# Optimization experiments

Measured on AMD Instinct MI355X. Metric: run time of the kernel, lower is better.

The kernel has to match this reference:

```python
import jax, jax.numpy as jnp
import numpy as np

B, C, H, W = 8, 512, 32, 32
NH, DH = 8, 64            # n_head, d_head = C // n_head
L = 2                     # n_layer
NC, DC = 77, 768          # n_cond, d_cond
GROUPS = 32


def _layernorm(x, s, b, eps=1e-5):
    mu = jnp.mean(x, axis=-1, keepdims=True)
    var = jnp.var(x, axis=-1, keepdims=True)
    return (x - mu) * jax.lax.rsqrt(var + eps) * s + b


def _groupnorm(x, s, b, eps=1e-6):
    # x: (B,C,H,W) -> 32 groups over channels
    b_, c_, h_, w_ = x.shape
    xg = x.reshape(b_, GROUPS, c_ // GROUPS, h_, w_)
    mu = jnp.mean(xg, axis=(2, 3, 4), keepdims=True)
    var = jnp.var(xg, axis=(2, 3, 4), keepdims=True)
    xg = (xg - mu) * jax.lax.rsqrt(var + eps)
    return xg.reshape(b_, c_, h_, w_) * s[None, :, None, None] + b[None, :, None, None]


def _attention(x, kv, wq, wk, wv, wo, bo):
    # NOTE: source's normal_attention applies NO 1/sqrt(d) scale (faithful).
    bsz, sq, _ = x.shape
    sk = kv.shape[1]
    q = (x @ wq).reshape(bsz, sq, NH, DH)
    k = (kv @ wk).reshape(bsz, sk, NH, DH)
    v = (kv @ wv).reshape(bsz, sk, NH, DH)
    attn = jnp.einsum('bind,bjnd->bnij', q, k)
    attn = jax.nn.softmax(attn, axis=-1)
    out = jnp.einsum('bnij,bjnd->bind', attn, v).reshape(bsz, sq, NH * DH)
    return out @ wo + bo


def setup_inputs() -> dict:
    key = jax.random.key(0)
    ks = iter(jax.random.split(key, 40))
    rn = lambda *shape: jax.random.normal(next(ks), shape, dtype=jnp.float32) * 0.02
    d = {
        'x': jax.random.normal(next(ks), (B, C, H, W), dtype=jnp.float32),
        'cond': jax.random.normal(next(ks), (B, NC, DC), dtype=jnp.float32),
        'gn_s': jnp.ones((C,), jnp.float32), 'gn_b': jnp.zeros((C,), jnp.float32),
        'pin_w': rn(C, C), 'pin_b': jnp.zeros((C,), jnp.float32),
        'pout_w': rn(C, C), 'pout_b': jnp.zeros((C,), jnp.float32),
        # per-layer (stacked along leading L dim)
        'ln1_s': jnp.ones((L, C), jnp.float32), 'ln1_b': jnp.zeros((L, C), jnp.float32),
        'sa_wq': rn(L, C, C), 'sa_wk': rn(L, C, C), 'sa_wv': rn(L, C, C),
        'sa_wo': rn(L, C, C), 'sa_bo': jnp.zeros((L, C), jnp.float32),
        'ln2_s': jnp.ones((L, C), jnp.float32), 'ln2_b': jnp.zeros((L, C), jnp.float32),
        'ca_wq': rn(L, C, C), 'ca_wk': rn(L, DC, C), 'ca_wv': rn(L, DC, C),
        'ca_wo': rn(L, C, C), 'ca_bo': jnp.zeros((L, C), jnp.float32),
        'ln3_s': jnp.ones((L, C), jnp.float32), 'ln3_b': jnp.zeros((L, C), jnp.float32),
        'ff_w1': rn(L, C, 8 * C), 'ff_b1': jnp.zeros((L, 8 * C), jnp.float32),
        'ff_w2': rn(L, 4 * C, C), 'ff_b2': jnp.zeros((L, C), jnp.float32),
    }
    return d


def reference(x, cond, gn_s, gn_b, pin_w, pin_b, pout_w, pout_b,
              ln1_s, ln1_b, sa_wq, sa_wk, sa_wv, sa_wo, sa_bo,
              ln2_s, ln2_b, ca_wq, ca_wk, ca_wv, ca_wo, ca_bo,
              ln3_s, ln3_b, ff_w1, ff_b1, ff_w2, ff_b2):
    b, c, h, w = x.shape
    x_in = x
    xn = _groupnorm(x, gn_s, gn_b)
    # 1x1 conv == per-pixel linear
    xn = jnp.einsum('bchw,cd->bdhw', xn, pin_w) + pin_b[None, :, None, None]
    t = xn.transpose(0, 2, 3, 1).reshape(b, h * w, c)  # b (h w) c
    for i in range(L):
        t = _attention(_layernorm(t, ln1_s[i], ln1_b[i]), _layernorm(t, ln1_s[i], ln1_b[i]),
                       sa_wq[i], sa_wk[i], sa_wv[i], sa_wo[i], sa_bo[i]) + t
        t = _attention(_layernorm(t, ln2_s[i], ln2_b[i]), cond,
                       ca_wq[i], ca_wk[i], ca_wv[i], ca_wo[i], ca_bo[i]) + t
        hgate = _layernorm(t, ln3_s[i], ln3_b[i]) @ ff_w1[i] + ff_b1[i]
        u, gate = jnp.split(hgate, 2, axis=-1)
        t = (u * jax.nn.gelu(gate, approximate=False)) @ ff_w2[i] + ff_b2[i] + t
    y = t.reshape(b, h, w, c).transpose(0, 3, 1, 2)
    y = jnp.einsum('bchw,cd->bdhw', y, pout_w) + pout_b[None, :, None, None]
    return y + x_in
```

## Files before the change

kernel.cpp:

```cpp
#include <hip/hip_runtime.h>
#include <math.h>

static constexpr int Bn  = 8;
static constexpr int Cn  = 512;
static constexpr int HWn = 1024;
static constexpr int Sn  = 1024;
static constexpr int NCn = 77;
static constexpr int NCp = 640;
static constexpr int DCn = 768;

typedef unsigned short u16;
typedef __attribute__((ext_vector_type(8))) short short8v;
typedef __attribute__((ext_vector_type(4))) float f32x4;
typedef __attribute__((ext_vector_type(8))) unsigned short u16x8;

__device__ __forceinline__ u16 f2b(float f) {
  unsigned u = __float_as_uint(f);
  return (u16)((u + 0x7fffu + ((u >> 16) & 1u)) >> 16);
}
__device__ __forceinline__ float b2f(u16 h) {
  return __uint_as_float(((unsigned)h) << 16);
}

#define GLDS16(gp, lp) __builtin_amdgcn_global_load_lds( \
    (const __attribute__((address_space(1))) void*)(gp),  \
    (__attribute__((address_space(3))) void*)(lp), 16, 0, 0)

__global__ __launch_bounds__(256) void w_cast_t(const float* __restrict__ in,
    u16* __restrict__ out, int K, int N)
{
  __shared__ float tile[32][33];
  int k0 = blockIdx.x * 32, n0 = blockIdx.y * 32;
  int px = threadIdx.x & 31, py = threadIdx.x >> 5;
  for (int yy = py; yy < 32; yy += 8)
    tile[yy][px] = in[(size_t)(k0 + yy) * N + n0 + px];
  __syncthreads();
  for (int yy = py; yy < 32; yy += 8)
    out[(size_t)(n0 + yy) * K + k0 + px] = f2b(tile[px][yy]);
}

__global__ __launch_bounds__(256) void cond_cast(const float* __restrict__ in,
    u16* __restrict__ out)
{
  int idx = blockIdx.x * 256 + threadIdx.x;
  int m = idx / DCn;
  out[idx] = (m < Bn * NCn) ? f2b(in[idx]) : (u16)0;
}

__global__ __launch_bounds__(256) void cast_f2b8(const float* __restrict__ in,
    u16* __restrict__ out)
{
  int i = blockIdx.x * 256 + threadIdx.x;
  const float4* p = (const float4*)(in + (size_t)i * 8);
  float4 a = p[0], b = p[1];
  u16x8 o;
  o[0] = f2b(a.x); o[1] = f2b(a.y); o[2] = f2b(a.z); o[3] = f2b(a.w);
  o[4] = f2b(b.x); o[5] = f2b(b.y); o[6] = f2b(b.z); o[7] = f2b(b.w);
  *(u16x8*)(out + (size_t)i * 8) = o;
}

__global__ __launch_bounds__(256) void gn_kernel(const float* __restrict__ x,
    const float* __restrict__ gs, const float* __restrict__ gb, float* __restrict__ out)
{
  int b = blockIdx.x >> 5, g = blockIdx.x & 31;
  const float* xp = x + ((size_t)b * Cn + g * 16) * HWn;
  float s = 0.f, ss = 0.f;
  for (int e = threadIdx.x; e < 16 * HWn; e += 256) {
    float v = xp[e];
    s += v; ss += v * v;
  }
  __shared__ float red[10];
  #pragma unroll
  for (int o = 32; o; o >>= 1) { s += __shfl_xor(s, o, 64); ss += __shfl_xor(ss, o, 64); }
  if ((threadIdx.x & 63) == 0) { red[threadIdx.x >> 6] = s; red[(threadIdx.x >> 6) + 4] = ss; }
  __syncthreads();
  if (threadIdx.x == 0) {
    float st  = red[0] + red[1] + red[2] + red[3];
    float sst = red[4] + red[5] + red[6] + red[7];
    float mu  = st * (1.f / 16384.f);
    red[8] = mu;
    red[9] = rsqrtf(sst * (1.f / 16384.f) - mu * mu + 1e-6f);
  }
  __syncthreads();
  float mu = red[8], inv = red[9];
  float* op = out + ((size_t)b * Cn + g * 16) * HWn;
  for (int e = threadIdx.x; e < 16 * HWn; e += 256) {
    int cl = e >> 10;
    op[e] = (xp[e] - mu) * inv * gs[g * 16 + cl] + gb[g * 16 + cl];
  }
}

__global__ __launch_bounds__(256) void gn_t_cast(const float* __restrict__ in,
    u16* __restrict__ out)
{
  __shared__ float tile[32][33];
  int p0 = blockIdx.x * 32, c0 = blockIdx.y * 32, b = blockIdx.z;
  int px = threadIdx.x & 31, py = threadIdx.x >> 5;
  for (int yy = py; yy < 32; yy += 8)
    tile[yy][px] = in[((size_t)b * Cn + c0 + yy) * HWn + p0 + px];
  __syncthreads();
  for (int yy = py; yy < 32; yy += 8)
    out[((size_t)b * HWn + p0 + yy) * Cn + c0 + px] = f2b(tile[px][yy]);
}

__global__ __launch_bounds__(256) void ln_kernel(const float* __restrict__ in,
    const float* __restrict__ s, const float* __restrict__ b, u16* __restrict__ out)
{
  int row  = blockIdx.x * 4 + (threadIdx.x >> 6);
  int lane = threadIdx.x & 63;
  const float* ip = in + (size_t)row * Cn + lane * 8;
  float4 v0 = *(const float4*)ip;
  float4 v1 = *(const float4*)(ip + 4);
  float sum = v0.x + v0.y + v0.z + v0.w + v1.x + v1.y + v1.z + v1.w;
  float ss  = v0.x*v0.x + v0.y*v0.y + v0.z*v0.z + v0.w*v0.w
            + v1.x*v1.x + v1.y*v1.y + v1.z*v1.z + v1.w*v1.w;
  #pragma unroll
  for (int o = 32; o; o >>= 1) { sum += __shfl_xor(sum, o, 64); ss += __shfl_xor(ss, o, 64); }
  float mu  = sum * (1.f / Cn);
  float inv = rsqrtf(ss * (1.f / Cn) - mu * mu + 1e-5f);
  const float4 s0 = *(const float4*)(s + lane * 8);
  const float4 s1 = *(const float4*)(s + lane * 8 + 4);
  const float4 b0 = *(const float4*)(b + lane * 8);
  const float4 b1 = *(const float4*)(b + lane * 8 + 4);
  u16x8 o;
  o[0] = f2b((v0.x - mu) * inv * s0.x + b0.x);
  o[1] = f2b((v0.y - mu) * inv * s0.y + b0.y);
  o[2] = f2b((v0.z - mu) * inv * s0.z + b0.z);
  o[3] = f2b((v0.w - mu) * inv * s0.w + b0.w);
  o[4] = f2b((v1.x - mu) * inv * s1.x + b1.x);
  o[5] = f2b((v1.y - mu) * inv * s1.y + b1.y);
  o[6] = f2b((v1.z - mu) * inv * s1.z + b1.z);
  o[7] = f2b((v1.w - mu) * inv * s1.w + b1.w);
  *(u16x8*)(out + (size_t)row * Cn + lane * 8) = o;
}

template<int EPI, int OUT>
__global__ __launch_bounds__(256) void gemm_mfma(const u16* __restrict__ A,
    const u16* __restrict__ Bt, const float* __restrict__ bias,
    const float* __restrict__ res, void* __restrict__ outp, int M, int K, int N)
{
  __shared__ __align__(16) u16 As[128 * 32];
  __shared__ __align__(16) u16 Bs[128 * 32];
  int tid = threadIdx.x, lane = tid & 63, wid = tid >> 6;
  int n0 = blockIdx.x * 128, m0 = blockIdx.y * 128;
  int wr = wid >> 1, wc = wid & 1;
  int r16 = lane & 15, q4 = lane >> 4;
  f32x4 acc[4][4] = {};
  for (int k0 = 0; k0 < K; k0 += 32) {
    #pragma unroll
    for (int i = 0; i < 2; i++) {
      int c = wid * 128 + i * 64 + lane;
      size_t ldso = (size_t)(wid * 2 + i) * 1024;
      GLDS16(A  + (size_t)(m0 + (c >> 2)) * K + k0 + (c & 3) * 8, (char*)As + ldso);
      GLDS16(Bt + (size_t)(n0 + (c >> 2)) * K + k0 + (c & 3) * 8, (char*)Bs + ldso);
    }
    __syncthreads();
    short8v a[4], b[4];
    #pragma unroll
    for (int m = 0; m < 4; m++)
      a[m] = *(const short8v*)((const char*)As + (wr * 64 + m * 16 + r16) * 64 + q4 * 16);
    #pragma unroll
    for (int n = 0; n < 4; n++)
      b[n] = *(const short8v*)((const char*)Bs + (wc * 64 + n * 16 + r16) * 64 + q4 * 16);
    #pragma unroll
    for (int m = 0; m < 4; m++)
      #pragma unroll
      for (int n = 0; n < 4; n++)
        acc[m][n] = __builtin_amdgcn_mfma_f32_16x16x32_bf16(a[m], b[n], acc[m][n], 0, 0, 0);
    __syncthreads();
  }
  #pragma unroll
  for (int m = 0; m < 4; m++) {
    int gm0 = m0 + wr * 64 + m * 16 + q4 * 4;
    #pragma unroll
    for (int n = 0; n < 4; n++) {
      int gc = n0 + wc * 64 + n * 16 + r16;
      float bv = (EPI >= 1) ? bias[gc] : 0.f;
      if (OUT == 2) {
        int bb = gm0 >> 10, s0 = gm0 & 1023;
        ushort4 pk;
        pk.x = f2b(acc[m][n][0] + bv);
        pk.y = f2b(acc[m][n][1] + bv);
        pk.z = f2b(acc[m][n][2] + bv);
        pk.w = f2b(acc[m][n][3] + bv);
        *(ushort4*)((u16*)outp + ((size_t)bb * Cn + gc) * (size_t)Sn + s0) = pk;
      } else {
        #pragma unroll
        for (int r = 0; r < 4; r++) {
          float v = acc[m][n][r] + bv;
          size_t oi = (size_t)(gm0 + r) * N + gc;
          if (EPI == 2) v += res[oi];
          if (OUT == 0) ((float*)outp)[oi] = v;
          else          ((u16*)outp)[oi]   = f2b(v);
        }
      }
    }
  }
}

__global__ __launch_bounds__(256) void ff_gate_mfma(const u16* __restrict__ A,
    const u16* __restrict__ W1t, const float* __restrict__ bias,
    u16* __restrict__ out, int M, int K)
{
  __shared__ __align__(16) u16 As[128 * 32];
  __shared__ __align__(16) u16 Bu[128 * 32];
  __shared__ __align__(16) u16 Bg[128 * 32];
  int tid = threadIdx.x, lane = tid & 63, wid = tid >> 6;
  int n0 = blockIdx.x * 128, m0 = blockIdx.y * 128;
  int wr = wid >> 1, wc = wid & 1;
  int r16 = lane & 15, q4 = lane >> 4;
  f32x4 au[4][4] = {}, ag[4][4] = {};
  for (int k0 = 0; k0 < K; k0 += 32) {
    #pragma unroll
    for (int i = 0; i < 2; i++) {
      int c = wid * 128 + i * 64 + lane;
      size_t ldso = (size_t)(wid * 2 + i) * 1024;
      int row = c >> 2, sub = (c & 3) * 8;
      GLDS16(A   + (size_t)(m0 + row) * K + k0 + sub,          (char*)As + ldso);
      GLDS16(W1t + (size_t)(n0 + row) * K + k0 + sub,          (char*)Bu + ldso);
      GLDS16(W1t + (size_t)(2048 + n0 + row) * K + k0 + sub,   (char*)Bg + ldso);
    }
    __syncthreads();
    short8v a[4], bu[4], bg[4];
    #pragma unroll
    for (int m = 0; m < 4; m++)
      a[m] = *(const short8v*)((const char*)As + (wr * 64 + m * 16 + r16) * 64 + q4 * 16);
    #pragma unroll
    for (int n = 0; n < 4; n++) {
      bu[n] = *(const short8v*)((const char*)Bu + (wc * 64 + n * 16 + r16) * 64 + q4 * 16);
      bg[n] = *(const short8v*)((const char*)Bg + (wc * 64 + n * 16 + r16) * 64 + q4 * 16);
    }
    #pragma unroll
    for (int m = 0; m < 4; m++)
      #pragma unroll
      for (int n = 0; n < 4; n++) {
        au[m][n] = __builtin_amdgcn_mfma_f32_16x16x32_bf16(a[m], bu[n], au[m][n], 0, 0, 0);
        ag[m][n] = __builtin_amdgcn_mfma_f32_16x16x32_bf16(a[m], bg[n], ag[m][n], 0, 0, 0);
      }
    __syncthreads();
  }
  #pragma unroll
  for (int m = 0; m < 4; m++) {
    int gm0 = m0 + wr * 64 + m * 16 + q4 * 4;
    #pragma unroll
    for (int n = 0; n < 4; n++) {
      int gc = n0 + wc * 64 + n * 16 + r16;
      float bu_ = bias[gc], bg_ = bias[2048 + gc];
      #pragma unroll
      for (int r = 0; r < 4; r++) {
        float u = au[m][n][r] + bu_;
        float g = ag[m][n][r] + bg_;
        float ge = 0.5f * g * (1.f + erff(g * 0.70710678118f));
        out[(size_t)(gm0 + r) * 2048 + gc] = f2b(u * ge);
      }
    }
  }
}

__global__ __launch_bounds__(256) void attn_self_mfma(const u16* __restrict__ q,
    const u16* __restrict__ k, const u16* __restrict__ vt, u16* __restrict__ o)
{
  __shared__ __align__(16) u16 Qs[64 * 64];
  __shared__ __align__(16) u16 Ks[2][64 * 64];
  __shared__ __align__(16) u16 Vs[2][64 * 64];
  __shared__ __align__(16) u16 Ps[4 * 16 * 64];
  int tid = threadIdx.x, lane = tid & 63, wid = tid >> 6;
  int r16 = lane & 15, q4 = lane >> 4;
  int qt = blockIdx.x & 15, h = (blockIdx.x >> 4) & 7, b = blockIdx.x >> 7;

  const u16* qg = q  + ((size_t)(b * Sn + qt * 64)) * Cn + h * 64;
  const u16* kg = k  + ((size_t)b * Sn) * Cn + h * 64;
  const u16* vg = vt + ((size_t)(b * Cn + h * 64)) * Sn;

  #define STAGE_T(dst, gbase, rs) do { \
    _Pragma("unroll") \
    for (int ii = 0; ii < 2; ii++) { \
      int rr = ii * 32 + wid * 8 + (lane >> 3); \
      GLDS16((gbase) + (size_t)rr * (rs) + (((lane & 7) ^ (rr & 7)) << 3), \
             (char*)(dst) + ii * 4096 + wid * 1024); \
    } \
  } while (0)

  STAGE_T(Qs, qg, Cn);
  STAGE_T(Ks[0], kg, Cn);
  STAGE_T(Vs[0], vg, Sn);
  __syncthreads();

  short8v aq[2];
  {
    int qrow = wid * 16 + r16, sx = r16 & 7;
    const char* base = (const char*)Qs + qrow * 128;
    aq[0] = *(const short8v*)(base + ((q4 ^ sx) << 4));
    aq[1] = *(const short8v*)(base + (((4 | q4) ^ sx) << 4));
  }

  float m_r[4] = {-1e30f, -1e30f, -1e30f, -1e30f};
  float l_r[4] = {0.f, 0.f, 0.f, 0.f};
  f32x4 acc_o[4] = {};
  int cur = 0;
  char* pwave = (char*)Ps + wid * 2048;

  for (int t = 0; t < 16; t++) {
    if (t < 15) {
      STAGE_T(Ks[cur ^ 1], kg + (size_t)(t + 1) * 64 * Cn, Cn);
      STAGE_T(Vs[cur ^ 1], vg + (t + 1) * 64, Sn);
    }
    f32x4 s4[4];
    #pragma unroll
    for (int n = 0; n < 4; n++) {
      int krow = n * 16 + r16, sx = r16 & 7;
      const char* base = (const char*)Ks[cur] + krow * 128;
      short8v b0 = *(const short8v*)(base + ((q4 ^ sx) << 4));
      short8v b1 = *(const short8v*)(base + (((4 | q4) ^ sx) << 4));
      f32x4 z = {0.f, 0.f, 0.f, 0.f};
      z = __builtin_amdgcn_mfma_f32_16x16x32_bf16(aq[0], b0, z, 0, 0, 0);
      s4[n] = __builtin_amdgcn_mfma_f32_16x16x32_bf16(aq[1], b1, z, 0, 0, 0);
    }
    #pragma unroll
    for (int r = 0; r < 4; r++) {
      float tm = fmaxf(fmaxf(s4[0][r], s4[1][r]), fmaxf(s4[2][r], s4[3][r]));
      #pragma unroll
      for (int off = 8; off; off >>= 1) tm = fmaxf(tm, __shfl_xor(tm, off, 64));
      float mn = fmaxf(m_r[r], tm);
      float al = __expf(m_r[r] - mn);
      m_r[r] = mn;
      int prow = q4 * 4 + r;
      char* pbase = pwave + prow * 128;
      int sx = (prow & 7) << 4;
      float rs = 0.f;
      #pragma unroll
      for (int n = 0; n < 4; n++) {
        float p = __expf(s4[n][r] - mn);
        rs += p;
        int cb = ((((n << 4) | r16) << 1) ^ sx);
        *(u16*)(pbase + cb) = f2b(p);
      }
      #pragma unroll
      for (int off = 8; off; off >>= 1) rs += __shfl_xor(rs, off, 64);
      l_r[r] = l_r[r] * al + rs;
      #pragma unroll
      for (int n = 0; n < 4; n++) acc_o[n][r] *= al;
    }
    __syncthreads();
    short8v pa0, pa1;
    {
      int sx = r16 & 7;
      const char* base = pwave + r16 * 128;
      pa0 = *(const short8v*)(base + ((q4 ^ sx) << 4));
      pa1 = *(const short8v*)(base + (((4 | q4) ^ sx) << 4));
    }
    #pragma unroll
    for (int n = 0; n < 4; n++) {
      int vrow = n * 16 + r16, sx = r16 & 7;
      const char* base = (const char*)Vs[cur] + vrow * 128;
      short8v v0 = *(const short8v*)(base + ((q4 ^ sx) << 4));
      short8v v1 = *(const short8v*)(base + (((4 | q4) ^ sx) << 4));
      acc_o[n] = __builtin_amdgcn_mfma_f32_16x16x32_bf16(pa0, v0, acc_o[n], 0, 0, 0);
      acc_o[n] = __builtin_amdgcn_mfma_f32_16x16x32_bf16(pa1, v1, acc_o[n], 0, 0, 0);
    }
    __syncthreads();
    cur ^= 1;
  }

  u16* ob = o + ((size_t)(b * Sn + qt * 64 + wid * 16 + q4 * 4)) * Cn + h * 64;
  #pragma unroll
  for (int r = 0; r < 4; r++) {
    float inv = 1.f / l_r[r];
    #pragma unroll
    for (int n = 0; n < 4; n++)
      ob[(size_t)r * Cn + n * 16 + r16] = f2b(acc_o[n][r] * inv);
  }
  #undef STAGE_T
}

__global__ __launch_bounds__(256) void vt_cross_k(const u16* __restrict__ v,
    u16* __restrict__ vt)
{
  int c = blockIdx.x * 256 + threadIdx.x;
  int b = blockIdx.y;
  u16* op = vt + ((size_t)b * Cn + c) * 96;
  for (int j = 0; j < 96; j++)
    op[j] = (j < NCn) ? v[((size_t)b * NCn + j) * Cn + c] : (u16)0;
}

__global__ __launch_bounds__(256) void attn_cross_mfma(const u16* __restrict__ q,
    const u16* __restrict__ k, const u16* __restrict__ vt, u16* __restrict__ o)
{
  __shared__ __align__(16) u16 Ps[4][16 * 104];
  int tid = threadIdx.x, lane = tid & 63, wid = tid >> 6;
  int r16 = lane & 15, q4 = lane >> 4;
  int qt = blockIdx.x & 15, h = (blockIdx.x >> 4) & 7, b = blockIdx.x >> 7;

  const u16* qg = q + ((size_t)(b * Sn + qt * 64 + wid * 16 + r16)) * Cn + h * 64 + q4 * 8;
  short8v aq0 = *(const short8v*)qg;
  short8v aq1 = *(const short8v*)(qg + 32);

  f32x4 s[6];
  #pragma unroll
  for (int n = 0; n < 6; n++) {
    const u16* kr = k + ((size_t)(b * NCn + n * 16 + r16)) * Cn + h * 64 + q4 * 8;
    short8v b0 = *(const short8v*)kr;
    short8v b1 = *(const short8v*)(kr + 32);
    f32x4 z = {0.f, 0.f, 0.f, 0.f};
    z = __builtin_amdgcn_mfma_f32_16x16x32_bf16(aq0, b0, z, 0, 0, 0);
    s[n] = __builtin_amdgcn_mfma_f32_16x16x32_bf16(aq1, b1, z, 0, 0, 0);
  }
  #pragma unroll
  for (int n = 0; n < 6; n++)
    if (n * 16 + r16 >= NCn) {
      s[n][0] = -1e30f; s[n][1] = -1e30f; s[n][2] = -1e30f; s[n][3] = -1e30f;
    }

  float l_r[4];
  u16* pw = &Ps[wid][0];
  #pragma unroll
  for (int r = 0; r < 4; r++) {
    float tm = -1e30f;
    #pragma unroll
    for (int n = 0; n < 6; n++) tm = fmaxf(tm, s[n][r]);
    #pragma unroll
    for (int off = 8; off; off >>= 1) tm = fmaxf(tm, __shfl_xor(tm, off, 64));
    int prow = q4 * 4 + r;
    float rs = 0.f;
    #pragma unroll
    for (int n = 0; n < 6; n++) {
      float p = __expf(s[n][r] - tm);
      rs += p;
      pw[prow * 104 + n * 16 + r16] = f2b(p);
    }
    #pragma unroll
    for (int off = 8; off; off >>= 1) rs += __shfl_xor(rs, off, 64);
    l_r[r] = rs;
  }
  __syncthreads();

  short8v pa[3];
  #pragma unroll
  for (int c = 0; c < 3; c++)
    pa[c] = *(const short8v*)(pw + r16 * 104 + c * 32 + q4 * 8);
  f32x4 acc[4] = {};
  #pragma unroll
  for (int n = 0; n < 4; n++) {
    const u16* vr = vt + ((size_t)(b * Cn + h * 64 + n * 16 + r16)) * 96;
    #pragma unroll
    for (int c = 0; c < 3; c++) {
      short8v bv = *(const short8v*)(vr + c * 32 + q4 * 8);
      acc[n] = __builtin_amdgcn_mfma_f32_16x16x32_bf16(pa[c], bv, acc[n], 0, 0, 0);
    }
  }

  u16* ob = o + ((size_t)(b * Sn + qt * 64 + wid * 16 + q4 * 4)) * Cn + h * 64;
  #pragma unroll
  for (int r = 0; r < 4; r++) {
    float inv = 1.f / l_r[r];
    #pragma unroll
    for (int n = 0; n < 4; n++)
      ob[(size_t)r * Cn + n * 16 + r16] = f2b(acc[n][r] * inv);
  }
}

__global__ __launch_bounds__(256) void trans_add(const float* __restrict__ tin,
    const float* __restrict__ pb, const float* __restrict__ xin, float* __restrict__ out)
{
  __shared__ float tile[32][33];
  int p0 = blockIdx.x * 32, d0 = blockIdx.y * 32, b = blockIdx.z;
  int px = threadIdx.x & 31, py = threadIdx.x >> 5;
  for (int yy = py; yy < 32; yy += 8)
    tile[yy][px] = tin[((size_t)b * HWn + p0 + yy) * Cn + d0 + px];
  __syncthreads();
  for (int yy = py; yy < 32; yy += 8) {
    int dd = d0 + yy;
    size_t oidx = ((size_t)b * Cn + dd) * HWn + p0 + px;
    out[oidx] = tile[px][yy] + pb[dd] + xin[oidx];
  }
}

extern "C" void kernel_launch(void* const* d_in, const int* in_sizes, int n_in,
                              void* d_out, int out_size, void* d_ws, size_t ws_size,
                              hipStream_t stream) {
  const float* x      = (const float*)d_in[0];
  const float* cond   = (const float*)d_in[1];
  const float* gn_s   = (const float*)d_in[2];
  const float* gn_b   = (const float*)d_in[3];
  const float* pin_w  = (const float*)d_in[4];
  const float* pin_b  = (const float*)d_in[5];
  const float* pout_w = (const float*)d_in[6];
  const float* pout_b = (const float*)d_in[7];
  const float* ln1_s  = (const float*)d_in[8];
  const float* ln1_b  = (const float*)d_in[9];
  const float* sa_wq  = (const float*)d_in[10];
  const float* sa_wk  = (const float*)d_in[11];
  const float* sa_wv  = (const float*)d_in[12];
  const float* sa_wo  = (const float*)d_in[13];
  const float* sa_bo  = (const float*)d_in[14];
  const float* ln2_s  = (const float*)d_in[15];
  const float* ln2_b  = (const float*)d_in[16];
  const float* ca_wq  = (const float*)d_in[17];
  const float* ca_wk  = (const float*)d_in[18];
  const float* ca_wv  = (const float*)d_in[19];
  const float* ca_wo  = (const float*)d_in[20];
  const float* ca_bo  = (const float*)d_in[21];
  const float* ln3_s  = (const float*)d_in[22];
  const float* ln3_b  = (const float*)d_in[23];
  const float* ff_w1  = (const float*)d_in[24];
  const float* ff_b1  = (const float*)d_in[25];
  const float* ff_w2  = (const float*)d_in[26];
  const float* ff_b2  = (const float*)d_in[27];

  const int M = Bn * Sn;
  const size_t MB = 1ull << 20;
  char* ws = (char*)d_ws;
  float* t     = (float*)(ws);
  u16*   abf   = (u16*)  (ws + 16 * MB);
  float* qb    = (float*)(ws + 24 * MB);
  float* kb    = (float*)(ws + 40 * MB);
  float* vb    = (float*)(ws + 56 * MB);
  u16*   hb    = (u16*)  (ws + 72 * MB);
  float* gnout = (float*)(ws + 72 * MB);
  u16*   xb    = (u16*)  (ws + 88 * MB);
  u16*   vtc   = (u16*)  (ws + 96 * MB);
  u16*   condb = (u16*)  (ws + 104 * MB);
  u16*   wts   = (u16*)  (ws + 105 * MB);

  u16* q16  = (u16*)qb;
  u16* k16  = (u16*)kb;
  u16* v16  = (u16*)vb;
  u16* vt16 = (u16*)vb;

  u16* wp = wts;
  u16* pinT  = wp; wp += 512 * 512;
  u16* poutT = wp; wp += 512 * 512;
  u16 *sa_wqT[2], *sa_wkT[2], *sa_wvT[2], *sa_woT[2];
  u16 *ca_wqT[2], *ca_wkT[2], *ca_wvT[2], *ca_woT[2], *ff_w1T[2], *ff_w2T[2];
  for (int i = 0; i < 2; i++) {
    sa_wqT[i] = wp; wp += 512 * 512;
    sa_wkT[i] = wp; wp += 512 * 512;
    sa_wvT[i] = wp; wp += 512 * 512;
    sa_woT[i] = wp; wp += 512 * 512;
    ca_wqT[i] = wp; wp += 512 * 512;
    ca_wkT[i] = wp; wp += 768 * 512;
    ca_wvT[i] = wp; wp += 768 * 512;
    ca_woT[i] = wp; wp += 512 * 512;
    ff_w1T[i] = wp; wp += 512 * 4096;
    ff_w2T[i] = wp; wp += 2048 * 512;
  }

  dim3 tcc(16, 16);
  w_cast_t<<<tcc, 256, 0, stream>>>(pin_w, pinT, 512, 512);
  w_cast_t<<<tcc, 256, 0, stream>>>(pout_w, poutT, 512, 512);
  for (int i = 0; i < 2; i++) {
    const size_t wCC = (size_t)i * 512 * 512, wDC = (size_t)i * 768 * 512;
    w_cast_t<<<tcc, 256, 0, stream>>>(sa_wq + wCC, sa_wqT[i], 512, 512);
    w_cast_t<<<tcc, 256, 0, stream>>>(sa_wk + wCC, sa_wkT[i], 512, 512);
    w_cast_t<<<tcc, 256, 0, stream>>>(sa_wv + wCC, sa_wvT[i], 512, 512);
    w_cast_t<<<tcc, 256, 0, stream>>>(sa_wo + wCC, sa_woT[i], 512, 512);
    w_cast_t<<<tcc, 256, 0, stream>>>(ca_wq + wCC, ca_wqT[i], 512, 512);
    w_cast_t<<<dim3(24, 16), 256, 0, stream>>>(ca_wk + wDC, ca_wkT[i], 768, 512);
    w_cast_t<<<dim3(24, 16), 256, 0, stream>>>(ca_wv + wDC, ca_wvT[i], 768, 512);
    w_cast_t<<<tcc, 256, 0, stream>>>(ca_wo + wCC, ca_woT[i], 512, 512);
    w_cast_t<<<dim3(16, 128), 256, 0, stream>>>(ff_w1 + (size_t)i * 512 * 4096, ff_w1T[i], 512, 4096);
    w_cast_t<<<dim3(64, 16), 256, 0, stream>>>(ff_w2 + (size_t)i * 2048 * 512, ff_w2T[i], 2048, 512);
  }
  cond_cast<<<(NCp * DCn) / 256, 256, 0, stream>>>(cond, condb);

  gn_kernel<<<256, 256, 0, stream>>>(x, gn_s, gn_b, gnout);
  gn_t_cast<<<dim3(32, 16, 8), 256, 0, stream>>>(gnout, xb);
  gemm_mfma<1, 0><<<dim3(4, 64), 256, 0, stream>>>(xb, pinT, pin_b, nullptr, t, M, 512, 512);

  for (int i = 0; i < 2; i++) {
    ln_kernel<<<2048, 256, 0, stream>>>(t, ln1_s + i * Cn, ln1_b + i * Cn, abf);
    gemm_mfma<0, 1><<<dim3(4, 64), 256, 0, stream>>>(abf, sa_wqT[i], nullptr, nullptr, q16, M, 512, 512);
    gemm_mfma<0, 1><<<dim3(4, 64), 256, 0, stream>>>(abf, sa_wkT[i], nullptr, nullptr, k16, M, 512, 512);
    gemm_mfma<0, 2><<<dim3(4, 64), 256, 0, stream>>>(abf, sa_wvT[i], nullptr, nullptr, vt16, M, 512, 512);
    attn_self_mfma<<<1024, 256, 0, stream>>>(q16, k16, vt16, abf);
    gemm_mfma<2, 0><<<dim3(4, 64), 256, 0, stream>>>(abf, sa_woT[i], sa_bo + i * Cn, t, t, M, 512, 512);
    ln_kernel<<<2048, 256, 0, stream>>>(t, ln2_s + i * Cn, ln2_b + i * Cn, abf);
    gemm_mfma<0, 1><<<dim3(4, 64), 256, 0, stream>>>(abf, ca_wqT[i], nullptr, nullptr, q16, M, 512, 512);
    gemm_mfma<0, 1><<<dim3(4, 5), 256, 0, stream>>>(condb, ca_wkT[i], nullptr, nullptr, k16, NCp, 768, 512);
    gemm_mfma<0, 1><<<dim3(4, 5), 256, 0, stream>>>(condb, ca_wvT[i], nullptr, nullptr, v16, NCp, 768, 512);
    vt_cross_k<<<dim3(2, 8), 256, 0, stream>>>(v16, vtc);
    attn_cross_mfma<<<1024, 256, 0, stream>>>(q16, k16, vtc, abf);
    gemm_mfma<2, 0><<<dim3(4, 64), 256, 0, stream>>>(abf, ca_woT[i], ca_bo + i * Cn, t, t, M, 512, 512);
    ln_kernel<<<2048, 256, 0, stream>>>(t, ln3_s + i * Cn, ln3_b + i * Cn, abf);
    ff_gate_mfma<<<dim3(16, 64), 256, 0, stream>>>(abf, ff_w1T[i], ff_b1 + i * 4096, hb, M, 512);
    gemm_mfma<2, 0><<<dim3(4, 64), 256, 0, stream>>>(hb, ff_w2T[i], ff_b2 + i * Cn, t, t, M, 2048, 512);
  }

  cast_f2b8<<<2048, 256, 0, stream>>>(t, xb);
  gemm_mfma<0, 0><<<dim3(4, 64), 256, 0, stream>>>(xb, poutT, nullptr, nullptr, qb, M, 512, 512);
  trans_add<<<dim3(32, 16, 8), 256, 0, stream>>>(qb, pout_b, x, (float*)d_out);
}
```

Baseline: 1.123 ms.

## Fuse QKV and cross-KV GEMMs, add 64-row tile variant, use fast erf

Merges the three self-attention projection GEMMs into one N=1536 launch whose epilogue routes columns to q, k and transposed v. It likewise merges the cross-attention K and V projections into one N=1024 launch. Both rely on the transposed weight buffers sitting contiguously in memory. The 512-wide GEMMs switch to a 64-row M tile, doubling the grid to better fill the CUs. The library erff in the GEGLU epilogue is replaced with an Abramowitz-Stegun polynomial plus exp, which adds a small approximation error.

```diff
diff --git a/kernel.cpp b/kernel.cpp
--- a/kernel.cpp
+++ b/kernel.cpp
@@ -20,6 +20,14 @@
 }
 __device__ __forceinline__ float b2f(u16 h) {
   return __uint_as_float(((unsigned)h) << 16);
+}
+__device__ __forceinline__ float erf_as(float x) {
+  float ax = fabsf(x);
+  float t  = 1.f / (1.f + 0.3275911f * ax);
+  float y  = t * (0.254829592f + t * (-0.284496736f + t * (1.421413741f +
+             t * (-1.453152027f + t * 1.061405429f))));
+  float r  = 1.f - y * __expf(-ax * ax);
+  return copysignf(r, x);
 }
 
 #define GLDS16(gp, lp) __builtin_amdgcn_global_load_lds( \
@@ -134,44 +142,57 @@
   *(u16x8*)(out + (size_t)row * Cn + lane * 8) = o;
 }
 
-template<int EPI, int OUT>
+template<int EPI, int OUT, int MT>
 __global__ __launch_bounds__(256) void gemm_mfma(const u16* __restrict__ A,
     const u16* __restrict__ Bt, const float* __restrict__ bias,
-    const float* __restrict__ res, void* __restrict__ outp, int M, int K, int N)
-{
-  __shared__ __align__(16) u16 As[128 * 32];
+    const float* __restrict__ res, void* __restrict__ outp,
+    void* __restrict__ out2, void* __restrict__ out3, int M, int K, int N)
+{
+  constexpr int MFR = MT / 32;
+  __shared__ __align__(16) u16 As[MT * 32];
   __shared__ __align__(16) u16 Bs[128 * 32];
   int tid = threadIdx.x, lane = tid & 63, wid = tid >> 6;
-  int n0 = blockIdx.x * 128, m0 = blockIdx.y * 128;
+  int n0 = blockIdx.x * 128, m0 = blockIdx.y * MT;
   int wr = wid >> 1, wc = wid & 1;
   int r16 = lane & 15, q4 = lane >> 4;
-  f32x4 acc[4][4] = {};
+  f32x4 acc[MFR][4] = {};
   for (int k0 = 0; k0 < K; k0 += 32) {
+    if (MT == 128) {
+      #pragma unroll
+      for (int i = 0; i < 2; i++) {
+        int c = wid * 128 + i * 64 + lane;
+        GLDS16(A + (size_t)(m0 + (c >> 2)) * K + k0 + (c & 3) * 8,
+               (char*)As + (size_t)(wid * 2 + i) * 1024);
+      }
+    } else {
+      int c = tid;
+      GLDS16(A + (size_t)(m0 + (c >> 2)) * K + k0 + (c & 3) * 8,
+             (char*)As + (size_t)wid * 1024);
+    }
     #pragma unroll
     for (int i = 0; i < 2; i++) {
       int c = wid * 128 + i * 64 + lane;
-      size_t ldso = (size_t)(wid * 2 + i) * 1024;
-      GLDS16(A  + (size_t)(m0 + (c >> 2)) * K + k0 + (c & 3) * 8, (char*)As + ldso);
-      GLDS16(Bt + (size_t)(n0 + (c >> 2)) * K + k0 + (c & 3) * 8, (char*)Bs + ldso);
+      GLDS16(Bt + (size_t)(n0 + (c >> 2)) * K + k0 + (c & 3) * 8,
+             (char*)Bs + (size_t)(wid * 2 + i) * 1024);
     }
     __syncthreads();
-    short8v a[4], b[4];
-    #pragma unroll
-    for (int m = 0; m < 4; m++)
-      a[m] = *(const short8v*)((const char*)As + (wr * 64 + m * 16 + r16) * 64 + q4 * 16);
+    short8v a[MFR], b[4];
+    #pragma unroll
+    for (int m = 0; m < MFR; m++)
+      a[m] = *(const short8v*)((const char*)As + (wr * (MT / 2) + m * 16 + r16) * 64 + q4 * 16);
     #pragma unroll
     for (int n = 0; n < 4; n++)
       b[n] = *(const short8v*)((const char*)Bs + (wc * 64 + n * 16 + r16) * 64 + q4 * 16);
     #pragma unroll
-    for (int m = 0; m < 4; m++)
+    for (int m = 0; m < MFR; m++)
       #pragma unroll
       for (int n = 0; n < 4; n++)
         acc[m][n] = __builtin_amdgcn_mfma_f32_16x16x32_bf16(a[m], b[n], acc[m][n], 0, 0, 0);
     __syncthreads();
   }
   #pragma unroll
-  for (int m = 0; m < 4; m++) {
-    int gm0 = m0 + wr * 64 + m * 16 + q4 * 4;
+  for (int m = 0; m < MFR; m++) {
+    int gm0 = m0 + wr * (MT / 2) + m * 16 + q4 * 4;
     #pragma unroll
     for (int n = 0; n < 4; n++) {
       int gc = n0 + wc * 64 + n * 16 + r16;
@@ -184,6 +205,26 @@
         pk.z = f2b(acc[m][n][2] + bv);
         pk.w = f2b(acc[m][n][3] + bv);
         *(ushort4*)((u16*)outp + ((size_t)bb * Cn + gc) * (size_t)Sn + s0) = pk;
+      } else if (OUT == 3) {
+        if (gc < 1024) {
+          u16* dst = (gc < 512) ? (u16*)outp : (u16*)out2;
+          int cc = gc & 511;
+          #pragma unroll
+          for (int r = 0; r < 4; r++)
+            dst[(size_t)(gm0 + r) * Cn + cc] = f2b(acc[m][n][r]);
+        } else {
+          int bb = gm0 >> 10, s0 = gm0 & 1023, cc = gc - 1024;
+          ushort4 pk;
+          pk.x = f2b(acc[m][n][0]); pk.y = f2b(acc[m][n][1]);
+          pk.z = f2b(acc[m][n][2]); pk.w = f2b(acc[m][n][3]);
+          *(ushort4*)((u16*)out3 + ((size_t)bb * Cn + cc) * (size_t)Sn + s0) = pk;
+        }
+      } else if (OUT == 4) {
+        u16* dst = (gc < 512) ? (u16*)outp : (u16*)out2;
+        int cc = gc & 511;
+        #pragma unroll
+        for (int r = 0; r < 4; r++)
+          dst[(size_t)(gm0 + r) * Cn + cc] = f2b(acc[m][n][r]);
       } else {
         #pragma unroll
         for (int r = 0; r < 4; r++) {
@@ -250,7 +291,7 @@
       for (int r = 0; r < 4; r++) {
         float u = au[m][n][r] + bu_;
         float g = ag[m][n][r] + bg_;
-        float ge = 0.5f * g * (1.f + erff(g * 0.70710678118f));
+        float ge = 0.5f * g * (1.f + erf_as(g * 0.70710678118f));
         out[(size_t)(gm0 + r) * 2048 + gc] = f2b(u * ge);
       }
     }
@@ -565,28 +606,25 @@
 
   gn_kernel<<<256, 256, 0, stream>>>(x, gn_s, gn_b, gnout);
   gn_t_cast<<<dim3(32, 16, 8), 256, 0, stream>>>(gnout, xb);
-  gemm_mfma<1, 0><<<dim3(4, 64), 256, 0, stream>>>(xb, pinT, pin_b, nullptr, t, M, 512, 512);
+  gemm_mfma<1, 0, 64><<<dim3(4, 128), 256, 0, stream>>>(xb, pinT, pin_b, nullptr, t, nullptr, nullptr, M, 512, 512);
 
   for (int i = 0; i < 2; i++) {
     ln_kernel<<<2048, 256, 0, stream>>>(t, ln1_s + i * Cn, ln1_b + i * Cn, abf);
-    gemm_mfma<0, 1><<<dim3(4, 64), 256, 0, stream>>>(abf, sa_wqT[i], nullptr, nullptr, q16, M, 512, 512);
-    gemm_mfma<0, 1><<<dim3(4, 64), 256, 0, stream>>>(abf, sa_wkT[i], nullptr, nullptr, k16, M, 512, 512);
-    gemm_mfma<0, 2><<<dim3(4, 64), 256, 0, stream>>>(abf, sa_wvT[i], nullptr, nullptr, vt16, M, 512, 512);
+    gemm_mfma<0, 3, 128><<<dim3(12, 64), 256, 0, stream>>>(abf, sa_wqT[i], nullptr, nullptr, q16, k16, vt16, M, 512, 1536);
     attn_self_mfma<<<1024, 256, 0, stream>>>(q16, k16, vt16, abf);
-    gemm_mfma<2, 0><<<dim3(4, 64), 256, 0, stream>>>(abf, sa_woT[i], sa_bo + i * Cn, t, t, M, 512, 512);
+    gemm_mfma<2, 0, 64><<<dim3(4, 128), 256, 0, stream>>>(abf, sa_woT[i], sa_bo + i * Cn, t, t, nullptr, nullptr, M, 512, 512);
     ln_kernel<<<2048, 256, 0, stream>>>(t, ln2_s + i * Cn, ln2_b + i * Cn, abf);
-    gemm_mfma<0, 1><<<dim3(4, 64), 256, 0, stream>>>(abf, ca_wqT[i], nullptr, nullptr, q16, M, 512, 512);
-    gemm_mfma<0, 1><<<dim3(4, 5), 256, 0, stream>>>(condb, ca_wkT[i], nullptr, nullptr, k16, NCp, 768, 512);
-    gemm_mfma<0, 1><<<dim3(4, 5), 256, 0, stream>>>(condb, ca_wvT[i], nullptr, nullptr, v16, NCp, 768, 512);
+    gemm_mfma<0, 1, 64><<<dim3(4, 128), 256, 0, stream>>>(abf, ca_wqT[i], nullptr, nullptr, q16, nullptr, nullptr, M, 512, 512);
+    gemm_mfma<0, 4, 128><<<dim3(8, 5), 256, 0, stream>>>(condb, ca_wkT[i], nullptr, nullptr, k16, v16, nullptr, NCp, 768, 1024);
     vt_cross_k<<<dim3(2, 8), 256, 0, stream>>>(v16, vtc);
     attn_cross_mfma<<<1024, 256, 0, stream>>>(q16, k16, vtc, abf);
-    gemm_mfma<2, 0><<<dim3(4, 64), 256, 0, stream>>>(abf, ca_woT[i], ca_bo + i * Cn, t, t, M, 512, 512);
+    gemm_mfma<2, 0, 64><<<dim3(4, 128), 256, 0, stream>>>(abf, ca_woT[i], ca_bo + i * Cn, t, t, nullptr, nullptr, M, 512, 512);
     ln_kernel<<<2048, 256, 0, stream>>>(t, ln3_s + i * Cn, ln3_b + i * Cn, abf);
     ff_gate_mfma<<<dim3(16, 64), 256, 0, stream>>>(abf, ff_w1T[i], ff_b1 + i * 4096, hb, M, 512);
-    gemm_mfma<2, 0><<<dim3(4, 64), 256, 0, stream>>>(hb, ff_w2T[i], ff_b2 + i * Cn, t, t, M, 2048, 512);
+    gemm_mfma<2, 0, 64><<<dim3(4, 128), 256, 0, stream>>>(hb, ff_w2T[i], ff_b2 + i * Cn, t, t, nullptr, nullptr, M, 2048, 512);
   }
 
   cast_f2b8<<<2048, 256, 0, stream>>>(t, xb);
-  gemm_mfma<0, 0><<<dim3(4, 64), 256, 0, stream>>>(xb, poutT, nullptr, nullptr, qb, M, 512, 512);
+  gemm_mfma<0, 0, 64><<<dim3(4, 128), 256, 0, stream>>>(xb, poutT, nullptr, nullptr, qb, nullptr, nullptr, M, 512, 512);
   trans_add<<<dim3(32, 16, 8), 256, 0, stream>>>(qb, pout_b, x, (float*)d_out);
 }
```

New measurement: 992.3 us. -11.6%, faster.
